# Kernel tuning notes

Hardware: AMD Instinct MI355X
Metric: run time of the kernel (lower is better)

Reference implementation:

```python
import jax, jax.numpy as jnp
import numpy as np

B, C, T, H, W, E, K = 2, 256, 16, 32, 32, 4, 2


def setup_inputs() -> dict:
    key = jax.random.key(0)
    ks = jax.random.split(key, 5)
    x = jax.random.normal(ks[0], (B, C, T, H, W), dtype=jnp.float32)
    # gate: Conv3d(dim, E, 1) -> weight [E, C], bias [E]
    gate_w = jax.random.normal(ks[1], (E, C), dtype=jnp.float32) * 0.02
    gate_b = jnp.zeros((E,), dtype=jnp.float32)
    # experts_layer1: Conv3d(dim, dim*E, 1) -> weight [E*C, C], bias [E*C]
    w1 = jax.random.normal(ks[2], (E * C, C), dtype=jnp.float32) * 0.02
    b1 = jnp.zeros((E * C,), dtype=jnp.float32)
    # experts_layer2: Conv3d(dim*E, dim*E, 1, groups=E) -> per-expert [C, C]
    w2 = jax.random.normal(ks[3], (E, C, C), dtype=jnp.float32) * 0.02
    b2 = jnp.zeros((E, C), dtype=jnp.float32)
    return {"x": x, "gate_w": gate_w, "gate_b": gate_b,
            "w1": w1, "b1": b1, "w2": w2, "b2": b2}


def reference(x, gate_w, gate_b, w1, b1, w2, b2):
    # gating: 1x1x1 conv == channel contraction; logits [B,T,H,W,E]
    logits = jnp.einsum('bcthw,ec->bthwe', x, gate_w) + gate_b
    vals, idx = jax.lax.top_k(logits, K)              # [B,T,H,W,K]
    wk = jax.nn.softmax(vals, axis=-1).astype(x.dtype)
    # scatter top-k softmax weights back into E slots (zeros elsewhere)
    weights = jnp.sum(jax.nn.one_hot(idx, E, dtype=x.dtype) * wk[..., None],
                      axis=-2)                        # [B,T,H,W,E]
    # layer1 (dense 1x1x1 conv) + SiLU; output channels = E*C
    h = jax.nn.silu(jnp.einsum('bcthw,oc->bothw', x, w1)
                    + b1[None, :, None, None, None])
    h = h.reshape(B, E, C, T, H, W)
    # layer2: grouped 1x1x1 conv, one [C,C] matmul per expert
    expert_out = (jnp.einsum('becthw,eoc->beothw', h, w2)
                  + b2[None, :, :, None, None, None])  # [B,E,C,T,H,W]
    # weighted combine over experts + residual
    out = jnp.einsum('becthw,bthwe->bcthw', expert_out, weights)
    return out + x
```

## Files before the change

### kernel.cpp

```cpp
#include <hip/hip_runtime.h>
#include <hip/hip_bf16.h>


#define C_DIM 256
#define S_DIM 16384
#define E_DIM 4
#define MT 64
#define XST 264
#define WFRAG_ELEMS 262144

typedef __attribute__((ext_vector_type(8))) short bf16x8;
typedef __attribute__((ext_vector_type(4))) float f32x4;

__device__ __forceinline__ short bfq(float f) {
  __hip_bfloat16 h = __float2bfloat16(f);
  return *(short*)&h;
}

__global__ __launch_bounds__(256) void prepack_kernel(
    const float* __restrict__ w1, const float* __restrict__ w2,
    __hip_bfloat16* __restrict__ dst)
{
  int o8   = blockIdx.x * 256 + threadIdx.x;
  int half = o8 >> 15;
  int idx  = o8 & 32767;
  int j    = idx & 31;
  int rowid= idx >> 5;
  int e    = rowid >> 8;
  int nt   = (rowid >> 4) & 15;
  int row  = rowid & 15;
  int kc   = j >> 2;
  int col8 = j & 3;
  int lane = (col8 << 4) | row;
  const float* src = half ? w2 : w1;
  const float* s = src + rowid * 256 + j * 8;
  const float4 v0 = *(const float4*)s;
  const float4 v1 = *(const float4*)(s + 4);
  bf16x8 outv = {bfq(v0.x), bfq(v0.y), bfq(v0.z), bfq(v0.w),
                 bfq(v1.x), bfq(v1.y), bfq(v1.z), bfq(v1.w)};
  int chunk = ((e*16 + nt)*8 + kc)*64 + lane;
  *(bf16x8*)((short*)dst + half*WFRAG_ELEMS + chunk*8) = outv;
}

template<int MTC>
__device__ __forceinline__ void gemm1_sparse(
    const short* XsS, short* HsS, const short* w1e, const float* b1e,
    const unsigned char* plist_e, const float* wgtg_e,
    int wv, int r, int q, bool dosync)
{
  f32x4 hacc[MTC][2];
#pragma unroll
  for (int i = 0; i < MTC; ++i)
#pragma unroll
    for (int j = 0; j < 2; ++j) hacc[i][j] = (f32x4){0.f, 0.f, 0.f, 0.f};

  int aoff[MTC];
#pragma unroll
  for (int Mt = 0; Mt < MTC; ++Mt)
    aoff[Mt] = (int)plist_e[Mt*16 + r] * XST;

  bf16x8 bw[2][2];
#pragma unroll
  for (int t = 0; t < 2; ++t) bw[0][t] = *(const bf16x8*)(w1e + (t*8 + 0)*512);
  __builtin_amdgcn_s_setprio(1);
#pragma unroll
  for (int kc = 0; kc < 8; ++kc) {
    if (kc < 7) {
#pragma unroll
      for (int t = 0; t < 2; ++t)
        bw[(kc+1)&1][t] = *(const bf16x8*)(w1e + (t*8 + kc + 1)*512);
    }
    bf16x8 a[MTC];
#pragma unroll
    for (int Mt = 0; Mt < MTC; ++Mt)
      a[Mt] = *(const bf16x8*)(XsS + aoff[Mt] + kc*32 + q*8);
#pragma unroll
    for (int Mt = 0; Mt < MTC; ++Mt)
#pragma unroll
      for (int t = 0; t < 2; ++t)
        hacc[Mt][t] = __builtin_amdgcn_mfma_f32_16x16x32_bf16(a[Mt], bw[kc&1][t], hacc[Mt][t], 0, 0, 0);
  }
  __builtin_amdgcn_s_setprio(0);

  if (dosync) __syncthreads();

#pragma unroll
  for (int Mt = 0; Mt < MTC; ++Mt) {
    const int g0 = Mt*16 + q*4;
    const unsigned pw = *(const unsigned*)(plist_e + g0);
    const f32x4 wg = *(const f32x4*)(wgtg_e + g0);
#pragma unroll
    for (int t = 0; t < 2; ++t) {
      const int n = wv*32 + t*16 + r;
      const float bias = b1e[n];
#pragma unroll
      for (int reg = 0; reg < 4; ++reg) {
        const int p = (pw >> (8*reg)) & 255;
        const float z = hacc[Mt][t][reg] + bias;
        const float s = __builtin_amdgcn_rcpf(1.0f + __expf(-z));
        HsS[p*XST + n] = bfq(z * s * wg[reg]);
      }
    }
  }
}

__global__ __launch_bounds__(512, 4) void moe_fused_kernel(
    const float* __restrict__ x,
    const float* __restrict__ gate_w,
    const float* __restrict__ gate_b,
    const float* __restrict__ b1,
    const float* __restrict__ b2,
    const __hip_bfloat16* __restrict__ wp,
    float* __restrict__ out)
{
  __shared__ __align__(16) char pool[2 * MT * XST * 2];
  __shared__ __align__(16) float Wgt[MT * 4];
  __shared__ __align__(16) unsigned char plist[4][64];
  __shared__ __align__(16) float WgtG[4][64];
  __shared__ __align__(4)  unsigned char zlist[4][64];
  __shared__ int mcnt[4];

  short* XsS = (short*)pool;
  short* HsS = (short*)(pool + MT * XST * 2);

  const int tid  = threadIdx.x;
  const int lane = tid & 63;
  const int wv   = tid >> 6;
  const int r    = lane & 15;
  const int q    = lane >> 4;

  const int g  = blockIdx.x;
  const int b  = g >> 8;
  const int s0 = (g & 255) * MT;
  const float* xb = x + (size_t)b * C_DIM * S_DIM + s0;

  const short* W1P = (const short*)wp;
  const short* W2P = (const short*)wp + WFRAG_ELEMS;

  {
    const int p  = lane;
    const int c0 = wv * 32;
    float xv[32];
#pragma unroll
    for (int j = 0; j < 32; ++j)
      xv[j] = xb[(size_t)(c0 + j) * S_DIM + p];

    double acc[4] = {0.0, 0.0, 0.0, 0.0};
#pragma unroll
    for (int j = 0; j < 32; ++j) {
      const double xd = (double)xv[j];
      acc[0] += xd * (double)gate_w[0*256 + c0 + j];
      acc[1] += xd * (double)gate_w[1*256 + c0 + j];
      acc[2] += xd * (double)gate_w[2*256 + c0 + j];
      acc[3] += xd * (double)gate_w[3*256 + c0 + j];
    }

#pragma unroll
    for (int k = 0; k < 4; ++k) {
      bf16x8 blk = {bfq(xv[k*8+0]), bfq(xv[k*8+1]), bfq(xv[k*8+2]), bfq(xv[k*8+3]),
                    bfq(xv[k*8+4]), bfq(xv[k*8+5]), bfq(xv[k*8+6]), bfq(xv[k*8+7])};
      *(bf16x8*)(XsS + p*XST + c0 + k*8) = blk;
    }

    double* GateD = (double*)HsS;
#pragma unroll
    for (int e = 0; e < 4; ++e)
      GateD[(e*8 + wv)*64 + p] = acc[e];
  }
  __syncthreads();

  if (tid < 256) {
    const int p = tid >> 2;
    const int e = tid & 3;
    const double* GateD = (const double*)HsS;
    double s = (double)gate_b[e];
#pragma unroll
    for (int g2 = 0; g2 < 8; ++g2) s += GateD[(e*8 + g2)*64 + p];
    const float la = (float)s;
    const float lb = __shfl_xor(la, 1, 64);
    const float lc = __shfl_xor(la, 2, 64);
    const float ld = __shfl_xor(lb, 2, 64);
    if (e == 0) {
      const float l0 = la, l1 = lb, l2 = lc, l3 = ld;
      int i1 = 0; float v1 = l0;
      if (l1 > v1) { v1 = l1; i1 = 1; }
      if (l2 > v1) { v1 = l2; i1 = 2; }
      if (l3 > v1) { v1 = l3; i1 = 3; }
      float v2 = -3.0e38f; int i2 = 0;
      if (i1 != 0 && l0 > v2) { v2 = l0; i2 = 0; }
      if (i1 != 1 && l1 > v2) { v2 = l1; i2 = 1; }
      if (i1 != 2 && l2 > v2) { v2 = l2; i2 = 2; }
      if (i1 != 3 && l3 > v2) { v2 = l3; i2 = 3; }
      const float wA = 1.0f / (1.0f + __expf(v2 - v1));
      const float wB = 1.0f - wA;
      f32x4 w;
      w[0] = (i1 == 0) ? wA : ((i2 == 0) ? wB : 0.0f);
      w[1] = (i1 == 1) ? wA : ((i2 == 1) ? wB : 0.0f);
      w[2] = (i1 == 2) ? wA : ((i2 == 2) ? wB : 0.0f);
      w[3] = (i1 == 3) ? wA : ((i2 == 3) ? wB : 0.0f);
      *(f32x4*)(&Wgt[p*4]) = w;
    }
  }
  __syncthreads();

  if (wv < 4) {
    const int e = wv;
    const int p = lane;
    const float w = Wgt[p*4 + e];
    const bool sel = (w != 0.0f);
    const unsigned long long mask = __ballot(sel);
    const int below = __popcll(mask & ((1ull << p) - 1ull));
    const int m = __popcll(mask);
    const int pad = (((m + 15) >> 4) << 4) - m;
    if (sel) {
      plist[e][below] = (unsigned char)p;
      WgtG[e][below]  = w;
    } else {
      const int zidx = p - below;
      zlist[e][zidx] = (unsigned char)p;
      if (zidx < pad) {
        plist[e][m + zidx] = (unsigned char)p;
        WgtG[e][m + zidx]  = 0.0f;
      }
    }
    if (p == 0) mcnt[e] = m;
  }
  __syncthreads();

  f32x4 oacc[4][2];
#pragma unroll
  for (int i = 0; i < 4; ++i)
#pragma unroll
    for (int j = 0; j < 2; ++j) oacc[i][j] = (f32x4){0.f, 0.f, 0.f, 0.f};

  for (int e = 0; e < E_DIM; ++e) {
    const int me = mcnt[e];
    const int mt = __builtin_amdgcn_readfirstlane((me + 15) >> 4);
    const short* w1e = W1P + ((e*16 + wv*2)*8)*512 + lane*8;
    const float* b1e = b1 + e*256;
    const bool dosync = (e > 0);

    if      (mt == 2) gemm1_sparse<2>(XsS, HsS, w1e, b1e, plist[e], WgtG[e], wv, r, q, dosync);
    else if (mt == 3) gemm1_sparse<3>(XsS, HsS, w1e, b1e, plist[e], WgtG[e], wv, r, q, dosync);
    else if (mt == 4) gemm1_sparse<4>(XsS, HsS, w1e, b1e, plist[e], WgtG[e], wv, r, q, dosync);
    else if (mt == 1) gemm1_sparse<1>(XsS, HsS, w1e, b1e, plist[e], WgtG[e], wv, r, q, dosync);
    else { if (dosync) __syncthreads(); }

    const short* w2e = W2P + ((e*16 + wv*2)*8)*512 + lane*8;
    bf16x8 cw[2][2];
#pragma unroll
    for (int t = 0; t < 2; ++t) cw[0][t] = *(const bf16x8*)(w2e + (t*8 + 0)*512);

    {
      const int zm = MT - me;
      const bf16x8 zz = {0,0,0,0,0,0,0,0};
      for (int i = tid; i < zm*32; i += 512) {
        const int row = zlist[e][i >> 5];
        *(bf16x8*)(HsS + row*XST + (i & 31)*8) = zz;
      }
    }
    __syncthreads();

    {
      __builtin_amdgcn_s_setprio(1);
#pragma unroll
      for (int kc = 0; kc < 8; ++kc) {
        if (kc < 7) {
#pragma unroll
          for (int t = 0; t < 2; ++t)
            cw[(kc+1)&1][t] = *(const bf16x8*)(w2e + (t*8 + kc + 1)*512);
        }
        bf16x8 a[4];
#pragma unroll
        for (int Mt = 0; Mt < 4; ++Mt)
          a[Mt] = *(const bf16x8*)(HsS + (Mt*16 + r)*XST + kc*32 + q*8);
#pragma unroll
        for (int Mt = 0; Mt < 4; ++Mt)
#pragma unroll
          for (int t = 0; t < 2; ++t)
            oacc[Mt][t] = __builtin_amdgcn_mfma_f32_16x16x32_bf16(a[Mt], cw[kc&1][t], oacc[Mt][t], 0, 0, 0);
      }
      __builtin_amdgcn_s_setprio(0);
    }
  }

  {
    float b2v[2][4];
#pragma unroll
    for (int t = 0; t < 2; ++t) {
      const int c = wv*32 + t*16 + r;
#pragma unroll
      for (int e = 0; e < 4; ++e) b2v[t][e] = b2[e*256 + c];
    }
    float* ob = out + (size_t)b * C_DIM * S_DIM + s0;
#pragma unroll
    for (int Mt = 0; Mt < 4; ++Mt) {
      const int pb = Mt*16 + q*4;
      f32x4 wv4[4];
#pragma unroll
      for (int reg = 0; reg < 4; ++reg)
        wv4[reg] = *(const f32x4*)(&Wgt[(pb + reg)*4]);
#pragma unroll
      for (int t = 0; t < 2; ++t) {
        const int c = wv*32 + t*16 + r;
        f32x4 v = oacc[Mt][t];
#pragma unroll
        for (int reg = 0; reg < 4; ++reg)
          v[reg] += wv4[reg][0]*b2v[t][0] + wv4[reg][1]*b2v[t][1]
                  + wv4[reg][2]*b2v[t][2] + wv4[reg][3]*b2v[t][3];
        const float4 xr = *(const float4*)(xb + (size_t)c*S_DIM + pb);
        float4 res;
        res.x = v[0] + xr.x; res.y = v[1] + xr.y;
        res.z = v[2] + xr.z; res.w = v[3] + xr.w;
        *(float4*)(ob + (size_t)c*S_DIM + pb) = res;
      }
    }
  }
}

extern "C" void kernel_launch(void* const* d_in, const int* in_sizes, int n_in,
                              void* d_out, int out_size, void* d_ws, size_t ws_size,
                              hipStream_t stream)
{
  (void)in_sizes; (void)n_in; (void)out_size; (void)ws_size;
  const float* x      = (const float*)d_in[0];
  const float* gate_w = (const float*)d_in[1];
  const float* gate_b = (const float*)d_in[2];
  const float* w1     = (const float*)d_in[3];
  const float* b1     = (const float*)d_in[4];
  const float* w2     = (const float*)d_in[5];
  const float* b2     = (const float*)d_in[6];
  float* out = (float*)d_out;
  __hip_bfloat16* wpack = (__hip_bfloat16*)d_ws;

  prepack_kernel<<<256, 256, 0, stream>>>(w1, w2, wpack);
  moe_fused_kernel<<<512, 512, 0, stream>>>(x, gate_w, gate_b, b1, b2, wpack, out);
}
```

Measured before the change: 128.7 us.

## Replace sparse per-expert token compaction with dense expert GEMM1 over all tokens

Removes the per-expert ballot/popcount compaction of selected tokens, the padded gather lists, and the zero-fill of unselected H rows. GEMM1 now always runs on all 64 tokens per expert, and gate weights of zero zero out the unselected rows. This drops a sync, the gather indirection and the branchy template dispatch, at the cost of about twice the GEMM1 MFMA work when top-2 of 4 experts is selected. Gate weights are stored expert-major so the epilogue reads contiguous vectors.

```diff
diff --git a/kernel.cpp b/kernel.cpp
--- a/kernel.cpp
+++ b/kernel.cpp
@@ -42,22 +42,15 @@
   *(bf16x8*)((short*)dst + half*WFRAG_ELEMS + chunk*8) = outv;
 }
 
-template<int MTC>
-__device__ __forceinline__ void gemm1_sparse(
+__device__ __forceinline__ void gemm1_dense(
     const short* XsS, short* HsS, const short* w1e, const float* b1e,
-    const unsigned char* plist_e, const float* wgtg_e,
-    int wv, int r, int q, bool dosync)
-{
-  f32x4 hacc[MTC][2];
-#pragma unroll
-  for (int i = 0; i < MTC; ++i)
+    const float* WgtE, int wv, int r, int q, bool dosync)
+{
+  f32x4 hacc[4][2];
+#pragma unroll
+  for (int i = 0; i < 4; ++i)
 #pragma unroll
     for (int j = 0; j < 2; ++j) hacc[i][j] = (f32x4){0.f, 0.f, 0.f, 0.f};
-
-  int aoff[MTC];
-#pragma unroll
-  for (int Mt = 0; Mt < MTC; ++Mt)
-    aoff[Mt] = (int)plist_e[Mt*16 + r] * XST;
 
   bf16x8 bw[2][2];
 #pragma unroll
@@ -70,12 +63,12 @@
       for (int t = 0; t < 2; ++t)
         bw[(kc+1)&1][t] = *(const bf16x8*)(w1e + (t*8 + kc + 1)*512);
     }
-    bf16x8 a[MTC];
-#pragma unroll
-    for (int Mt = 0; Mt < MTC; ++Mt)
-      a[Mt] = *(const bf16x8*)(XsS + aoff[Mt] + kc*32 + q*8);
-#pragma unroll
-    for (int Mt = 0; Mt < MTC; ++Mt)
+    bf16x8 a[4];
+#pragma unroll
+    for (int Mt = 0; Mt < 4; ++Mt)
+      a[Mt] = *(const bf16x8*)(XsS + (Mt*16 + r)*XST + kc*32 + q*8);
+#pragma unroll
+    for (int Mt = 0; Mt < 4; ++Mt)
 #pragma unroll
       for (int t = 0; t < 2; ++t)
         hacc[Mt][t] = __builtin_amdgcn_mfma_f32_16x16x32_bf16(a[Mt], bw[kc&1][t], hacc[Mt][t], 0, 0, 0);
@@ -85,17 +78,15 @@
   if (dosync) __syncthreads();
 
 #pragma unroll
-  for (int Mt = 0; Mt < MTC; ++Mt) {
-    const int g0 = Mt*16 + q*4;
-    const unsigned pw = *(const unsigned*)(plist_e + g0);
-    const f32x4 wg = *(const f32x4*)(wgtg_e + g0);
+  for (int Mt = 0; Mt < 4; ++Mt) {
+    const f32x4 wg = *(const f32x4*)(WgtE + Mt*16 + q*4);
 #pragma unroll
     for (int t = 0; t < 2; ++t) {
       const int n = wv*32 + t*16 + r;
       const float bias = b1e[n];
 #pragma unroll
       for (int reg = 0; reg < 4; ++reg) {
-        const int p = (pw >> (8*reg)) & 255;
+        const int p = Mt*16 + q*4 + reg;
         const float z = hacc[Mt][t][reg] + bias;
         const float s = __builtin_amdgcn_rcpf(1.0f + __expf(-z));
         HsS[p*XST + n] = bfq(z * s * wg[reg]);
@@ -114,11 +105,7 @@
     float* __restrict__ out)
 {
   __shared__ __align__(16) char pool[2 * MT * XST * 2];
-  __shared__ __align__(16) float Wgt[MT * 4];
-  __shared__ __align__(16) unsigned char plist[4][64];
-  __shared__ __align__(16) float WgtG[4][64];
-  __shared__ __align__(4)  unsigned char zlist[4][64];
-  __shared__ int mcnt[4];
+  __shared__ __align__(16) float Wgt[4][MT];
 
   short* XsS = (short*)pool;
   short* HsS = (short*)(pool + MT * XST * 2);
@@ -193,40 +180,14 @@
       if (i1 != 3 && l3 > v2) { v2 = l3; i2 = 3; }
       const float wA = 1.0f / (1.0f + __expf(v2 - v1));
       const float wB = 1.0f - wA;
-      f32x4 w;
-      w[0] = (i1 == 0) ? wA : ((i2 == 0) ? wB : 0.0f);
-      w[1] = (i1 == 1) ? wA : ((i2 == 1) ? wB : 0.0f);
-      w[2] = (i1 == 2) ? wA : ((i2 == 2) ? wB : 0.0f);
-      w[3] = (i1 == 3) ? wA : ((i2 == 3) ? wB : 0.0f);
-      *(f32x4*)(&Wgt[p*4]) = w;
+      Wgt[0][p] = (i1 == 0) ? wA : ((i2 == 0) ? wB : 0.0f);
+      Wgt[1][p] = (i1 == 1) ? wA : ((i2 == 1) ? wB : 0.0f);
+      Wgt[2][p] = (i1 == 2) ? wA : ((i2 == 2) ? wB : 0.0f);
+      Wgt[3][p] = (i1 == 3) ? wA : ((i2 == 3) ? wB : 0.0f);
     }
   }
   __syncthreads();
 
-  if (wv < 4) {
-    const int e = wv;
-    const int p = lane;
-    const float w = Wgt[p*4 + e];
-    const bool sel = (w != 0.0f);
-    const unsigned long long mask = __ballot(sel);
-    const int below = __popcll(mask & ((1ull << p) - 1ull));
-    const int m = __popcll(mask);
-    const int pad = (((m + 15) >> 4) << 4) - m;
-    if (sel) {
-      plist[e][below] = (unsigned char)p;
-      WgtG[e][below]  = w;
-    } else {
-      const int zidx = p - below;
-      zlist[e][zidx] = (unsigned char)p;
-      if (zidx < pad) {
-        plist[e][m + zidx] = (unsigned char)p;
-        WgtG[e][m + zidx]  = 0.0f;
-      }
-    }
-    if (p == 0) mcnt[e] = m;
-  }
-  __syncthreads();
-
   f32x4 oacc[4][2];
 #pragma unroll
   for (int i = 0; i < 4; ++i)
@@ -234,31 +195,16 @@
     for (int j = 0; j < 2; ++j) oacc[i][j] = (f32x4){0.f, 0.f, 0.f, 0.f};
 
   for (int e = 0; e < E_DIM; ++e) {
-    const int me = mcnt[e];
-    const int mt = __builtin_amdgcn_readfirstlane((me + 15) >> 4);
     const short* w1e = W1P + ((e*16 + wv*2)*8)*512 + lane*8;
-    const float* b1e = b1 + e*256;
     const bool dosync = (e > 0);
 
-    if      (mt == 2) gemm1_sparse<2>(XsS, HsS, w1e, b1e, plist[e], WgtG[e], wv, r, q, dosync);
-    else if (mt == 3) gemm1_sparse<3>(XsS, HsS, w1e, b1e, plist[e], WgtG[e], wv, r, q, dosync);
-    else if (mt == 4) gemm1_sparse<4>(XsS, HsS, w1e, b1e, plist[e], WgtG[e], wv, r, q, dosync);
-    else if (mt == 1) gemm1_sparse<1>(XsS, HsS, w1e, b1e, plist[e], WgtG[e], wv, r, q, dosync);
-    else { if (dosync) __syncthreads(); }
+    gemm1_dense(XsS, HsS, w1e, b1 + e*256, &Wgt[e][0], wv, r, q, dosync);
 
     const short* w2e = W2P + ((e*16 + wv*2)*8)*512 + lane*8;
     bf16x8 cw[2][2];
 #pragma unroll
     for (int t = 0; t < 2; ++t) cw[0][t] = *(const bf16x8*)(w2e + (t*8 + 0)*512);
 
-    {
-      const int zm = MT - me;
-      const bf16x8 zz = {0,0,0,0,0,0,0,0};
-      for (int i = tid; i < zm*32; i += 512) {
-        const int row = zlist[e][i >> 5];
-        *(bf16x8*)(HsS + row*XST + (i & 31)*8) = zz;
-      }
-    }
     __syncthreads();
 
     {
@@ -296,18 +242,18 @@
 #pragma unroll
     for (int Mt = 0; Mt < 4; ++Mt) {
       const int pb = Mt*16 + q*4;
-      f32x4 wv4[4];
-#pragma unroll
-      for (int reg = 0; reg < 4; ++reg)
-        wv4[reg] = *(const f32x4*)(&Wgt[(pb + reg)*4]);
+      f32x4 wge[4];
+#pragma unroll
+      for (int e = 0; e < 4; ++e)
+        wge[e] = *(const f32x4*)(&Wgt[e][pb]);
 #pragma unroll
       for (int t = 0; t < 2; ++t) {
         const int c = wv*32 + t*16 + r;
         f32x4 v = oacc[Mt][t];
 #pragma unroll
         for (int reg = 0; reg < 4; ++reg)
-          v[reg] += wv4[reg][0]*b2v[t][0] + wv4[reg][1]*b2v[t][1]
-                  + wv4[reg][2]*b2v[t][2] + wv4[reg][3]*b2v[t][3];
+          v[reg] += wge[0][reg]*b2v[t][0] + wge[1][reg]*b2v[t][1]
+                  + wge[2][reg]*b2v[t][2] + wge[3][reg]*b2v[t][3];
         const float4 xr = *(const float4*)(xb + (size_t)c*S_DIM + pb);
         float4 res;
         res.x = v[0] + xr.x; res.y = v[1] + xr.y;
```

New measurement: 130.7 us. No clear change (+1.6%).
